# Kernel optimization log

Hardware: AMD Instinct MI355X
Metric: run time of the kernel (lower is better)

Reference implementation:

```python
import jax, jax.numpy as jnp
import numpy as np

IMG_H = IMG_W = 2048
N_LEVELS = 16
N_FEAT = 2
LOG2_T = 19
T = 1 << LOG2_T  # 524288 hash table entries per level
BASE = 16.0
FINEST = 2048.0
P1 = np.uint32(2654435761)  # second spatial-hash prime (first prime is 1)
MASK = np.uint32(T - 1)
OFFSETS = jnp.array([[0, 0], [0, 1], [1, 0], [1, 1]], dtype=jnp.int32)


def _resolutions():
    # matches torch float32 arithmetic: b = exp((ln finest - ln base)/(L-1))
    b = np.float32(np.exp((np.log(np.float32(FINEST)) - np.log(np.float32(BASE))) / (N_LEVELS - 1)))
    return [int(np.floor(np.float32(BASE) * b ** np.float32(i))) for i in range(N_LEVELS)]

RES = _resolutions()


def _sorted_vertex_hashes(res):
    # hash_integer over the full (res+1)x(res+1) vertex grid, sorted -> the consistent-hash ring.
    g = np.arange(res + 1, dtype=np.uint32)
    h = (g[:, None] ^ (g[None, :] * P1)) & MASK  # uint32 wraps, low 19 bits identical to int64 torch
    return np.sort(h.ravel()).astype(np.int32)

# Only levels whose dense grid exceeds the hash table use consistent hashing.
SORTED = {i: jnp.asarray(_sorted_vertex_hashes(RES[i]))
          for i in range(N_LEVELS) if (RES[i] + 1) ** 2 > T}


def setup_inputs() -> dict:
    key = jax.random.key(0)
    k1, k2 = jax.random.split(key)
    B = 1 << 21  # ~2.1M query points
    x = jax.random.uniform(k1, (B, 2), dtype=jnp.float32) * jnp.array([IMG_H, IMG_W], jnp.float32)
    tables = jax.random.uniform(k2, (N_LEVELS, T, N_FEAT), dtype=jnp.float32,
                                minval=-1e-4, maxval=1e-4)
    return {"x": x, "tables": tables}


def _level_embed(x, table, level):
    res = RES[level]
    gs = jnp.array([IMG_H / res, IMG_W / res], jnp.float32)  # [y_grid_size, x_grid_size]
    bl = jnp.floor(x / gs).astype(jnp.int32)                 # bottom-left cell index, [B,2]
    gmin = bl.astype(jnp.float32) * gs
    gmax = gmin + gs
    corners = bl[:, None, :] + OFFSETS[None]                 # [B,4,2] four cell corners
    if (res + 1) ** 2 <= T:
        idx = corners[..., 0] * res + corners[..., 1]        # one-to-one hash
    else:
        # spatial hash, then consistent-hash ring lookup. The torch code adds a
        # fractional hash in (0,1) and searches radian keys (h'+1)*delta; since all
        # keys/queries are integer grid hashes this reduces exactly to: first table
        # entry >= h (and h is always present, so value == h pre-densify).
        h = ((corners[..., 0].astype(jnp.uint32)
              ^ (corners[..., 1].astype(jnp.uint32) * P1)) & MASK).astype(jnp.int32)
        tab = SORTED[level]
        idx = tab[jnp.searchsorted(tab, h)]                  # [B,4]
    emb = table[idx]                                         # [B,4,F] gather
    w = (x - gmin) / (gmax - gmin)                           # bilinear weights, [B,2]
    w0 = w[:, 0:1]
    w1 = w[:, 1:2]
    c0 = emb[:, 0] * (1 - w1) + emb[:, 1] * w1
    c1 = emb[:, 2] * (1 - w1) + emb[:, 3] * w1
    return c0 * (1 - w0) + c1 * w0                           # [B,F]


def reference(x, tables):
    outs = [_level_embed(x, tables[i], i) for i in range(N_LEVELS)]
    return jnp.concatenate(outs, axis=-1)                    # [B, N_LEVELS*N_FEAT]
```

## Files before the change

### kernel.cpp

```cpp
#include <hip/hip_runtime.h>
#include <cstdint>

#define TSIZE (1u << 19)
#define MASKU (TSIZE - 1u)
#define P1U 2654435761u

#define CBINS_X 128
#define NCHILD (CBINS_X * CBINS_X)
#define XPART 8
#define CAPX 32
#define SLOTS ((size_t)XPART * NCHILD * CAPX)

__device__ __forceinline__ void embed_point(float2 xv, int orig,
                                            const float* __restrict__ tables,
                                            float* __restrict__ out) {
  constexpr int RESV[16] = {16, 22, 30, 42, 58, 80, 111, 153,
                            212, 294, 406, 561, 776, 1072, 1482, 2047};
  const float2* tabs = reinterpret_cast<const float2*>(tables);

  float w0a[16], w1a[16];
  int baseA[12];
  uint32_t hidx[4][4];

#pragma unroll
  for (int l = 0; l < 16; ++l) {
    const int res = RESV[l];
    const float gs = (float)(2048.0 / (double)res);
    const float inv = (float)res * 0.00048828125f;
    float f0 = floorf(xv.x * inv);
    float f1 = floorf(xv.y * inv);
    float g0 = f0 * gs;
    float g1 = f1 * gs;
    w0a[l] = (xv.x - g0) * inv;
    w1a[l] = (xv.y - g1) * inv;
    if (l < 12) {
      baseA[l] = (int)f0 * res + (int)f1;
    } else {
      uint32_t u0 = (uint32_t)(int)f0;
      uint32_t u1m = (uint32_t)(int)f1 * P1U;
      hidx[l - 12][0] = (u0 ^ u1m) & MASKU;
      hidx[l - 12][1] = (u0 ^ (u1m + P1U)) & MASKU;
      hidx[l - 12][2] = ((u0 + 1u) ^ u1m) & MASKU;
      hidx[l - 12][3] = ((u0 + 1u) ^ (u1m + P1U)) & MASKU;
    }
  }

  float2 eh[4][4];
#pragma unroll
  for (int l = 0; l < 4; ++l) {
    const float2* tab = tabs + (size_t)(12 + l) * TSIZE;
    eh[l][0] = tab[hidx[l][0]];
    eh[l][1] = tab[hidx[l][1]];
    eh[l][2] = tab[hidx[l][2]];
    eh[l][3] = tab[hidx[l][3]];
  }
  float4 lo[12], hi[12];
#pragma unroll
  for (int l = 0; l < 12; ++l) {
    const float2* tab = tabs + (size_t)l * TSIZE;
    lo[l] = *reinterpret_cast<const float4*>(tab + baseA[l]);
    hi[l] = *reinterpret_cast<const float4*>(tab + baseA[l] + RESV[l]);
  }

  __builtin_amdgcn_sched_barrier(0);

  float feat[32];
#pragma unroll
  for (int l = 0; l < 12; ++l) {
    float w0 = w0a[l], w1 = w1a[l];
    float omw0 = 1.0f - w0, omw1 = 1.0f - w1;
    float c0x = lo[l].x * omw1 + lo[l].z * w1;
    float c0y = lo[l].y * omw1 + lo[l].w * w1;
    float c1x = hi[l].x * omw1 + hi[l].z * w1;
    float c1y = hi[l].y * omw1 + hi[l].w * w1;
    feat[2 * l]     = c0x * omw0 + c1x * w0;
    feat[2 * l + 1] = c0y * omw0 + c1y * w0;
  }
#pragma unroll
  for (int l = 0; l < 4; ++l) {
    float w0 = w0a[12 + l], w1 = w1a[12 + l];
    float omw0 = 1.0f - w0, omw1 = 1.0f - w1;
    float c0x = eh[l][0].x * omw1 + eh[l][1].x * w1;
    float c0y = eh[l][0].y * omw1 + eh[l][1].y * w1;
    float c1x = eh[l][2].x * omw1 + eh[l][3].x * w1;
    float c1y = eh[l][2].y * omw1 + eh[l][3].y * w1;
    feat[24 + 2 * l]     = c0x * omw0 + c1x * w0;
    feat[24 + 2 * l + 1] = c0y * omw0 + c1y * w0;
  }

  float4* o = reinterpret_cast<float4*>(out) + (size_t)orig * 8;
#pragma unroll
  for (int j = 0; j < 8; ++j) {
    o[j] = make_float4(feat[4 * j], feat[4 * j + 1], feat[4 * j + 2], feat[4 * j + 3]);
  }
}


__device__ __forceinline__ int child_of(float2 xv) {
  int bx = min((int)(xv.x * 0.0625f), CBINS_X - 1);
  int by = min((int)(xv.y * 0.0625f), CBINS_X - 1);
  int parent = ((bx >> 1) << 6) + (by >> 1);
  int quad = ((bx & 1) << 1) + (by & 1);
  return (parent << 2) + quad;
}

__global__ __launch_bounds__(256) void scatter_px(
    const float2* __restrict__ xs, int* __restrict__ cnt,
    float4* __restrict__ recs,
    int* __restrict__ ovf, int* __restrict__ ovf_cnt, int B) {
  int p = blockIdx.x * 256 + threadIdx.x;
  if (p >= B) return;
  int part = blockIdx.x & 7;
  float2 xv = xs[p];
  int pc = part * NCHILD + child_of(xv);
  int pos = atomicAdd(&cnt[pc], 1);
  if (pos < CAPX) {
    recs[(size_t)pc * CAPX + pos] =
        make_float4(xv.x, xv.y, __int_as_float(p), 0.0f);
  } else {
    int o = atomicAdd(ovf_cnt, 1);
    ovf[o] = p;
  }
}

__global__ __launch_bounds__(256, 1) void hashenc_cmp(
    const float4* __restrict__ recs, const int* __restrict__ cnt,
    const float* __restrict__ tables, float* __restrict__ out) {
  __shared__ int pre[9];
  int bid = blockIdx.x;
  int nb = gridDim.x;
  int chunk = nb >> 3;
  int child = (bid & 7) * chunk + (bid >> 3);
  if (threadIdx.x == 0) {
    int s = 0;
    pre[0] = 0;
#pragma unroll
    for (int k = 0; k < XPART; ++k) {
      s += min(cnt[k * NCHILD + child], CAPX);
      pre[k + 1] = s;
    }
  }
  __syncthreads();
  int total = pre[8];
  int i = threadIdx.x;
  if (i >= total) return;
  int k = 0;
#pragma unroll
  for (int kk = 1; kk < XPART; ++kk) k = (i >= pre[kk]) ? kk : k;
  int j = i - pre[k];
  float4 r = recs[((size_t)(k * NCHILD + child)) * CAPX + j];
  embed_point(make_float2(r.x, r.y), __float_as_int(r.z), tables, out);
}

__global__ __launch_bounds__(256) void ovf_kernel(
    const float2* __restrict__ xs, const int* __restrict__ ovf,
    const int* __restrict__ ovf_cnt, const float* __restrict__ tables,
    float* __restrict__ out) {
  int n = *ovf_cnt;
  for (int i = blockIdx.x * 256 + threadIdx.x; i < n; i += gridDim.x * 256) {
    int p = ovf[i];
    embed_point(xs[p], p, tables, out);
  }
}


__global__ __launch_bounds__(256, 2) void hashenc_plain(
    const float2* __restrict__ xs, const float* __restrict__ tables,
    float* __restrict__ out, int B) {
  int p = blockIdx.x * 256 + threadIdx.x;
  if (p >= B) return;
  embed_point(xs[p], p, tables, out);
}


extern "C" void kernel_launch(void* const* d_in, const int* in_sizes, int n_in,
                              void* d_out, int out_size, void* d_ws, size_t ws_size,
                              hipStream_t stream) {
  const float2* xs = (const float2*)d_in[0];
  const float* tables = (const float*)d_in[1];
  float* out = (float*)d_out;
  int B = in_sizes[0] / 2;
  int blocks = (B + 255) / 256;
  char* ws = (char*)d_ws;

  size_t c_recs = 0;
  size_t c_ovf = c_recs + SLOTS * 16;
  size_t c_cnt = c_ovf + (size_t)B * 4;
  size_t c_ocnt = c_cnt + (size_t)XPART * NCHILD * 4;
  size_t need = c_ocnt + 64;

  bool grid_ok = (blocks & 7) == 0;
  if (grid_ok && ws_size >= need) {
    float4* recs = (float4*)(ws + c_recs);
    int* ovf = (int*)(ws + c_ovf);
    int* cnt = (int*)(ws + c_cnt);
    int* ovf_cnt = (int*)(ws + c_ocnt);
    (void)hipMemsetAsync(cnt, 0, (size_t)XPART * NCHILD * 4 + 64, stream);
    hipLaunchKernelGGL(scatter_px, dim3(blocks), dim3(256), 0, stream,
                       xs, cnt, recs, ovf, ovf_cnt, B);
    hipLaunchKernelGGL(hashenc_cmp, dim3(NCHILD), dim3(256), 0, stream,
                       recs, cnt, tables, out);
    hipLaunchKernelGGL(ovf_kernel, dim3(32), dim3(256), 0, stream,
                       xs, ovf, ovf_cnt, tables, out);
  } else {
    hipLaunchKernelGGL(hashenc_plain, dim3(blocks), dim3(256), 0, stream,
                       xs, tables, out, B);
  }
}
```

Measured before the change: 268.3 us.

## Stage output features in LDS and write them cooperatively per wavefront

In the binned compute kernel, each thread now writes its 32 output features to a padded LDS buffer. Each wavefront then transposes them so groups of four lanes write one point's 128-byte output row as float4 stores, with the destination index shared via ds_bpermute. Before, every thread issued eight strided 16-byte stores to scattered rows. This is meant to make global writes more coalesced, at the cost of about 33KB of shared memory per block and extra LDS traffic. Reading shared memory within the wavefront with no barrier relies on wavefront lockstep, and there is no block-level sync.

```diff
diff --git a/kernel.cpp b/kernel.cpp
--- a/kernel.cpp
+++ b/kernel.cpp
@@ -11,9 +11,9 @@
 #define CAPX 32
 #define SLOTS ((size_t)XPART * NCHILD * CAPX)
 
-__device__ __forceinline__ void embed_point(float2 xv, int orig,
-                                            const float* __restrict__ tables,
-                                            float* __restrict__ out) {
+__device__ __forceinline__ void embed_core(float2 xv,
+                                           const float* __restrict__ tables,
+                                           float* __restrict__ feat) {
   constexpr int RESV[16] = {16, 22, 30, 42, 58, 80, 111, 153,
                             212, 294, 406, 561, 776, 1072, 1482, 2047};
   const float2* tabs = reinterpret_cast<const float2*>(tables);
@@ -64,7 +64,6 @@
 
   __builtin_amdgcn_sched_barrier(0);
 
-  float feat[32];
 #pragma unroll
   for (int l = 0; l < 12; ++l) {
     float w0 = w0a[l], w1 = w1a[l];
@@ -87,7 +86,13 @@
     feat[24 + 2 * l]     = c0x * omw0 + c1x * w0;
     feat[24 + 2 * l + 1] = c0y * omw0 + c1y * w0;
   }
-
+}
+
+__device__ __forceinline__ void embed_point(float2 xv, int orig,
+                                            const float* __restrict__ tables,
+                                            float* __restrict__ out) {
+  float feat[32];
+  embed_core(xv, tables, feat);
   float4* o = reinterpret_cast<float4*>(out) + (size_t)orig * 8;
 #pragma unroll
   for (int j = 0; j < 8; ++j) {
@@ -127,6 +132,7 @@
     const float4* __restrict__ recs, const int* __restrict__ cnt,
     const float* __restrict__ tables, float* __restrict__ out) {
   __shared__ int pre[9];
+  __shared__ float sf[256 * 33];
   int bid = blockIdx.x;
   int nb = gridDim.x;
   int chunk = nb >> 3;
@@ -142,14 +148,45 @@
   }
   __syncthreads();
   int total = pre[8];
-  int i = threadIdx.x;
-  if (i >= total) return;
-  int k = 0;
-#pragma unroll
-  for (int kk = 1; kk < XPART; ++kk) k = (i >= pre[kk]) ? kk : k;
-  int j = i - pre[k];
-  float4 r = recs[((size_t)(k * NCHILD + child)) * CAPX + j];
-  embed_point(make_float2(r.x, r.y), __float_as_int(r.z), tables, out);
+  int wbase = threadIdx.x & ~63;
+  if (wbase >= total) return;
+  int lane = threadIdx.x & 63;
+  int nact = min(total - wbase, 64);
+  bool active = lane < nact;
+
+  float feat[32];
+  int orig = 0;
+  if (active) {
+    int i = threadIdx.x;
+    int k = 0;
+#pragma unroll
+    for (int kk = 1; kk < XPART; ++kk) k = (i >= pre[kk]) ? kk : k;
+    int j = i - pre[k];
+    float4 r = recs[((size_t)(k * NCHILD + child)) * CAPX + j];
+    orig = __float_as_int(r.z);
+    embed_core(make_float2(r.x, r.y), tables, feat);
+  }
+
+  float* myf = &sf[threadIdx.x * 33];
+#pragma unroll
+  for (int f = 0; f < 32; ++f) myf[f] = feat[f];
+  __builtin_amdgcn_sched_barrier(0);
+
+  float* wf = &sf[wbase * 33];
+  int sub = lane & 3;
+#pragma unroll
+  for (int jj = 0; jj < 4; ++jj) {
+    int p = jj * 16 + (lane >> 2);
+    int op = __builtin_amdgcn_ds_bpermute(p << 2, orig);
+    if (p < nact) {
+#pragma unroll
+      for (int h = 0; h < 2; ++h) {
+        const float* src = &wf[p * 33 + h * 16 + sub * 4];
+        float4 v = make_float4(src[0], src[1], src[2], src[3]);
+        *reinterpret_cast<float4*>(out + (size_t)op * 32 + h * 16 + sub * 4) = v;
+      }
+    }
+  }
 }
 
 __global__ __launch_bounds__(256) void ovf_kernel(
```

Measured after the change: 239.5 us (median of 2 runs). 10.8% less time.
